# Performance work log

Hardware: AMD Instinct MI355X
Metric: run time of the kernel (lower is better)

Reference implementation:

```python
import jax, jax.numpy as jnp
import numpy as np

BETA_MAX = 0.01
CD_WEIGHT = 1.0
FIDELITY_WEIGHT = 0.5
BETA = BETA_MAX  # fully annealed (step >= beta_warmup)
EPS = 1e-12


def _pairwise_dist(a, b):
    """Euclidean distance matrix. a: [B,N,3], b: [B,M,3] -> [B,N,M]."""
    a2 = jnp.sum(a * a, axis=-1)                      # [B,N]
    b2 = jnp.sum(b * b, axis=-1)                      # [B,M]
    ab = jnp.einsum('bnd,bmd->bnm', a, b)             # [B,N,M]
    sq = a2[:, :, None] + b2[:, None, :] - 2.0 * ab
    return jnp.sqrt(jnp.maximum(sq, EPS))


def chamfer_distance_l1(pred, full):
    d = _pairwise_dist(pred, full)                    # [B,N,M]
    d_pf = jnp.min(d, axis=2)                         # pred -> full, [B,N]
    d_fp = jnp.min(d, axis=1)                         # full -> pred, [B,M]
    return 0.5 * (jnp.mean(d_pf) + jnp.mean(d_fp))


def fidelity_loss(partial, pred):
    # one-directional: every partial point should have a close predicted point
    d = _pairwise_dist(partial, pred)                 # [B,P,N]
    return jnp.mean(jnp.min(d, axis=2))


def kl_divergence(mu, logvar):
    # -0.5 * E_batch[ sum_dim (1 + logvar - mu^2 - exp(logvar)) ]
    kl = -0.5 * jnp.sum(1.0 + logvar - mu * mu - jnp.exp(logvar), axis=1)
    return jnp.mean(kl)


def setup_inputs() -> dict:
    key = jax.random.key(0)
    k1, k2, k3, k4, k5 = jax.random.split(key, 5)
    B, N, P, D = 8, 8192, 2048, 512
    return {
        'pred': jax.random.normal(k1, (B, N, 3), dtype=jnp.float32),
        'full': jax.random.normal(k2, (B, N, 3), dtype=jnp.float32),
        'partial': jax.random.normal(k3, (B, P, 3), dtype=jnp.float32),
        'mu': jax.random.normal(k4, (B, D), dtype=jnp.float32),
        'logvar': jax.random.normal(k5, (B, D), dtype=jnp.float32) * 0.1,
    }


def reference(pred, full, partial, mu, logvar):
    cd = chamfer_distance_l1(pred, full)
    kl = kl_divergence(mu, logvar)
    fidel = fidelity_loss(partial, pred)
    total = CD_WEIGHT * cd + BETA * kl + FIDELITY_WEIGHT * fidel
    return (total, cd, kl, fidel)
```

## Files before the change

### kernel.cpp

```cpp
#include <hip/hip_runtime.h>
#include <math.h>

#define BATCH 8
#define NPTS  8192
#define PPTS  2048
#define DLAT  512

typedef __attribute__((ext_vector_type(8)))  short short8;
typedef __attribute__((ext_vector_type(16))) float floatx16;

#define SEG      (2 * BATCH * NPTS + BATCH * PPTS)
#define DIR_PF   0
#define DIR_FP   (BATCH * NPTS)
#define DIR_FID  (2 * BATCH * NPTS)
#define OFF_SEG  8

#define CHUNK  1024
#define XBLK   512

__device__ __forceinline__ unsigned short f2bf(float f) {
    unsigned int u = __float_as_uint(f);
    return (unsigned short)((u + 0x7FFFu + ((u >> 16) & 1u)) >> 16);
}
__device__ __forceinline__ float bf2f(unsigned short s) {
    return __uint_as_float(((unsigned int)s) << 16);
}

__device__ __forceinline__ float min16(floatx16 d, float prev) {
    float a0 = fminf(fminf(d[0],  d[1]),  d[2]);
    float a1 = fminf(fminf(d[3],  d[4]),  d[5]);
    float a2 = fminf(fminf(d[6],  d[7]),  d[8]);
    float a3 = fminf(fminf(d[9],  d[10]), d[11]);
    float a4 = fminf(fminf(d[12], d[13]), d[14]);
    float b0 = fminf(fminf(a0, a1), a2);
    float b1 = fminf(fminf(a3, a4), d[15]);
    return fminf(fminf(b0, b1), prev);
}

__device__ __forceinline__ void encodeY(float y0, float y1, float y2,
                                        uint4* r0, uint4* r1) {
    const unsigned short h0 = f2bf(y0), h1 = f2bf(y1), h2 = f2bf(y2);
    const unsigned short l0 = f2bf(y0 - bf2f(h0));
    const unsigned short l1 = f2bf(y1 - bf2f(h1));
    const unsigned short l2 = f2bf(y2 - bf2f(h2));
    const float yn = fmaf(y0, y0, fmaf(y1, y1, y2 * y2));
    const unsigned short nh = f2bf(yn);
    const unsigned short nl = f2bf(yn - bf2f(nh));
    r0->x = (unsigned int)h0 | ((unsigned int)h1 << 16);
    r0->y = (unsigned int)h2 | ((unsigned int)l0 << 16);
    r0->z = (unsigned int)l1 | ((unsigned int)l2 << 16);
    r0->w = (unsigned int)h0 | ((unsigned int)h1 << 16);
    r1->x = (unsigned int)h2 | ((unsigned int)nh << 16);
    r1->y = (unsigned int)nl;
    r1->z = 0u; r1->w = 0u;
}

__global__ __launch_bounds__(256, 3) void minpass_kernel(
        const float* __restrict__ pred,
        const float* __restrict__ full,
        const float* __restrict__ partial,
        float* __restrict__ wsf,
        int ysplit) {
    const int bid = blockIdx.x;
    const int ys  = bid % ysplit;
    const int r   = bid / ysplit;
    const int b   = r / 36;
    const int s   = r % 36;
    const int yhalf = NPTS / ysplit;

    const int t = threadIdx.x;

    if (bid == 0) {
        if (t < 4) wsf[t] = 0.0f;
        if (t == 4) ((unsigned int*)wsf)[4] = 0u;
    }

    const float* xset; const float* yset; int minoff; int xbase;
    if (s < 16)      { xset = pred;    yset = full; xbase = b*NPTS + s*XBLK;
                       minoff = OFF_SEG + ys*SEG + DIR_PF  + b*NPTS + s*XBLK; }
    else if (s < 32) { xset = full;    yset = pred; xbase = b*NPTS + (s-16)*XBLK;
                       minoff = OFF_SEG + ys*SEG + DIR_FP  + b*NPTS + (s-16)*XBLK; }
    else             { xset = partial; yset = pred; xbase = b*PPTS + (s-32)*XBLK;
                       minoff = OFF_SEG + ys*SEG + DIR_FID + b*PPTS + (s-32)*XBLK; }

    const int lane = t & 63;
    const int wid  = t >> 6;
    const int l31  = lane & 31;
    const int half = lane >> 5;

    __shared__ uint4 sY[2][CHUNK];
    __shared__ uint4 sX[2][XBLK];
    __shared__ float sXn[XBLK];

    for (int i = t; i < XBLK; i += 256) {
        const float* xp = xset + (size_t)(xbase + i) * 3;
        const float x0 = xp[0], x1 = xp[1], x2 = xp[2];
        const float m0 = -2.0f*x0, m1 = -2.0f*x1, m2 = -2.0f*x2;
        const unsigned short h0 = f2bf(m0), h1 = f2bf(m1), h2 = f2bf(m2);
        const unsigned short l0 = f2bf(m0 - bf2f(h0));
        const unsigned short l1 = f2bf(m1 - bf2f(h1));
        const unsigned short l2 = f2bf(m2 - bf2f(h2));
        const unsigned int one = 0x3F80u;
        uint4 r0, r1;
        r0.x = (unsigned int)h0 | ((unsigned int)h1 << 16);
        r0.y = (unsigned int)h2 | ((unsigned int)h0 << 16);
        r0.z = (unsigned int)h1 | ((unsigned int)h2 << 16);
        r0.w = (unsigned int)l0 | ((unsigned int)l1 << 16);
        r1.x = (unsigned int)l2 | (one << 16);
        r1.y = one;
        r1.z = 0u; r1.w = 0u;
        sX[0][i] = r0; sX[1][i] = r1;
        sXn[i] = fmaf(x0, x0, fmaf(x1, x1, x2 * x2));
    }

    {
        const float* ypts = yset + (size_t)(b * NPTS + ys * yhalf) * 3;
        for (int i = t; i < CHUNK; i += 256) {
            const float* yp = ypts + (size_t)i * 3;
            uint4 r0, r1;
            encodeY(yp[0], yp[1], yp[2], &r0, &r1);
            sY[0][i] = r0; sY[1][i] = r1;
        }
    }
    __syncthreads();

    const int xw = wid * 128;
    const short8 bf0 = *(const short8*)&sX[half][xw + l31];
    const short8 bf1 = *(const short8*)&sX[half][xw + 32 + l31];
    const short8 bf2 = *(const short8*)&sX[half][xw + 64 + l31];
    const short8 bf3 = *(const short8*)&sX[half][xw + 96 + l31];
    const float  xn0 = sXn[xw + l31];
    const float  xn1 = sXn[xw + 32 + l31];
    const float  xn2 = sXn[xw + 64 + l31];
    const float  xn3 = sXn[xw + 96 + l31];

    const floatx16 zc = {0,0,0,0, 0,0,0,0, 0,0,0,0, 0,0,0,0};
    float cmin0 = 3.4e38f, cmin1 = 3.4e38f, cmin2 = 3.4e38f, cmin3 = 3.4e38f;

    const uint4* sYh = &sY[half][0];
    short8 af = *(const short8*)&sYh[l31];
#pragma unroll 4
    for (int j = 0; j < CHUNK / 32; ++j) {
        const short8 afn = *(const short8*)&sYh[((j + 1) & (CHUNK/32 - 1)) * 32 + l31];
        const floatx16 d0 = __builtin_amdgcn_mfma_f32_32x32x16_bf16(af, bf0, zc, 0, 0, 0);
        const floatx16 d1 = __builtin_amdgcn_mfma_f32_32x32x16_bf16(af, bf1, zc, 0, 0, 0);
        cmin0 = min16(d0, cmin0);
        const floatx16 d2 = __builtin_amdgcn_mfma_f32_32x32x16_bf16(af, bf2, zc, 0, 0, 0);
        cmin1 = min16(d1, cmin1);
        const floatx16 d3 = __builtin_amdgcn_mfma_f32_32x32x16_bf16(af, bf3, zc, 0, 0, 0);
        cmin2 = min16(d2, cmin2);
        cmin3 = min16(d3, cmin3);
        af = afn;
    }

    const float m0 = fminf(cmin0, __shfl_xor(cmin0, 32, 64));
    const float m1 = fminf(cmin1, __shfl_xor(cmin1, 32, 64));
    const float m2 = fminf(cmin2, __shfl_xor(cmin2, 32, 64));
    const float m3 = fminf(cmin3, __shfl_xor(cmin3, 32, 64));
    if (lane < 32) {
        wsf[minoff + xw + l31]      = fmaxf(m0 + xn0, 0.0f);
        wsf[minoff + xw + 32 + l31] = fmaxf(m1 + xn1, 0.0f);
        wsf[minoff + xw + 64 + l31] = fmaxf(m2 + xn2, 0.0f);
        wsf[minoff + xw + 96 + l31] = fmaxf(m3 + xn3, 0.0f);
    }
}

__device__ __forceinline__ float waveReduceSum(float v) {
#pragma unroll
    for (int o = 32; o > 0; o >>= 1) v += __shfl_down(v, o, 64);
    return v;
}

__device__ __forceinline__ float blockReduceSum(float v) {
    __shared__ float wsum[4];
    const int lane = threadIdx.x & 63;
    const int wid  = threadIdx.x >> 6;
    v = waveReduceSum(v);
    if (lane == 0) wsum[wid] = v;
    __syncthreads();
    if (wid == 0) {
        v = (lane < ((int)blockDim.x >> 6)) ? wsum[lane] : 0.0f;
        v = waveReduceSum(v);
    }
    return v;
}

#define NRED_BLOCKS 145
__global__ __launch_bounds__(256) void reduce_finalize_kernel(
        float* __restrict__ wsf,
        const float* __restrict__ mu,
        const float* __restrict__ logvar,
        float* __restrict__ out,
        int ysplit) {
    float* acc = wsf;
    unsigned int* cnt = (unsigned int*)wsf + 4;
    const int bid = blockIdx.x;
    const int t   = threadIdx.x;

    float v = 0.0f;
    int accIdx;
    if (bid < 144) {
        int base;
        if (bid < 64)       { accIdx = 0; base = DIR_PF  + bid * 1024;         }
        else if (bid < 128) { accIdx = 1; base = DIR_FP  + (bid - 64) * 1024;  }
        else                { accIdx = 2; base = DIR_FID + (bid - 128) * 1024; }
#pragma unroll
        for (int k = 0; k < 4; ++k) {
            const int i = OFF_SEG + base + k * 256 + t;
            float m = wsf[i];
            for (int sg = 1; sg < ysplit; ++sg) m = fminf(m, wsf[sg * SEG + i]);
            v += sqrtf(fmaxf(m, 1e-12f));
        }
    } else {
        accIdx = 3;
#pragma unroll
        for (int k = 0; k < BATCH * DLAT / 256; ++k) {
            const int i = k * 256 + t;
            const float m = mu[i];
            const float l = logvar[i];
            v += -0.5f * (1.0f + l - m * m - expf(l));
        }
    }

    v = blockReduceSum(v);
    if (t == 0) {
        atomicAdd(&acc[accIdx], v);
        __threadfence();
        const unsigned int done = atomicAdd(cnt, 1u);
        if (done == NRED_BLOCKS - 1) {
            const float s_pf  = atomicAdd(&acc[0], 0.0f);
            const float s_fp  = atomicAdd(&acc[1], 0.0f);
            const float s_fid = atomicAdd(&acc[2], 0.0f);
            const float s_kl  = atomicAdd(&acc[3], 0.0f);
            const float cd  = 0.5f * (s_pf / (float)(BATCH * NPTS) +
                                      s_fp / (float)(BATCH * NPTS));
            const float fid = s_fid / (float)(BATCH * PPTS);
            const float kl  = s_kl / (float)BATCH;
            out[0] = cd + 0.01f * kl + 0.5f * fid;
            out[1] = cd;
            out[2] = kl;
            out[3] = fid;
        }
    }
}

extern "C" void kernel_launch(void* const* d_in, const int* in_sizes, int n_in,
                              void* d_out, int out_size, void* d_ws, size_t ws_size,
                              hipStream_t stream) {
    const float* pred    = (const float*)d_in[0];
    const float* full    = (const float*)d_in[1];
    const float* partial = (const float*)d_in[2];
    const float* mu      = (const float*)d_in[3];
    const float* logvar  = (const float*)d_in[4];
    float* out = (float*)d_out;
    float* wsf = (float*)d_ws;

    int ysplit = 2;
    if (ws_size >= (size_t)(OFF_SEG + 8 * SEG) * 4) ysplit = 8;
    else if (ws_size >= (size_t)(OFF_SEG + 4 * SEG) * 4) ysplit = 4;

    minpass_kernel<<<8 * 36 * ysplit, 256, 0, stream>>>(pred, full, partial, wsf, ysplit);

    reduce_finalize_kernel<<<NRED_BLOCKS, 256, 0, stream>>>(wsf, mu, logvar, out, ysplit);
}
```

Before: 109.7 us.

## Switch to 16x16x32 bf16 MFMA with 8 x-tiles per wave and y-chunk loop

Replaces the 32x32x16 MFMA tiling with 16x16x32 MFMAs. Each wave now holds 8 x-fragments of 16 points, and the low-order bf16 terms are packed into the second K half so all 32 K slots carry data. The y dimension is now processed in a loop over CHUNK-sized tiles with syncs, so ysplit can be smaller than NPTS/CHUNK and more y work is done per block. The min reduction takes 4 outputs per MFMA instead of 16, which lowers the reduction VALU work per MFMA. The cost is more MFMA issues, zero-padded lanes for quads 2 and 3, and extra barriers per chunk.

```diff
diff --git a/kernel.cpp b/kernel.cpp
--- a/kernel.cpp
+++ b/kernel.cpp
@@ -6,8 +6,8 @@
 #define PPTS  2048
 #define DLAT  512
 
-typedef __attribute__((ext_vector_type(8)))  short short8;
-typedef __attribute__((ext_vector_type(16))) float floatx16;
+typedef __attribute__((ext_vector_type(8))) short short8;
+typedef __attribute__((ext_vector_type(4))) float floatx4;
 
 #define SEG      (2 * BATCH * NPTS + BATCH * PPTS)
 #define DIR_PF   0
@@ -26,16 +26,6 @@
     return __uint_as_float(((unsigned int)s) << 16);
 }
 
-__device__ __forceinline__ float min16(floatx16 d, float prev) {
-    float a0 = fminf(fminf(d[0],  d[1]),  d[2]);
-    float a1 = fminf(fminf(d[3],  d[4]),  d[5]);
-    float a2 = fminf(fminf(d[6],  d[7]),  d[8]);
-    float a3 = fminf(fminf(d[9],  d[10]), d[11]);
-    float a4 = fminf(fminf(d[12], d[13]), d[14]);
-    float b0 = fminf(fminf(a0, a1), a2);
-    float b1 = fminf(fminf(a3, a4), d[15]);
-    return fminf(fminf(b0, b1), prev);
-}
 
 __device__ __forceinline__ void encodeY(float y0, float y1, float y2,
                                         uint4* r0, uint4* r1) {
@@ -51,8 +41,9 @@
     r0->z = (unsigned int)l1 | ((unsigned int)l2 << 16);
     r0->w = (unsigned int)h0 | ((unsigned int)h1 << 16);
     r1->x = (unsigned int)h2 | ((unsigned int)nh << 16);
-    r1->y = (unsigned int)nl;
-    r1->z = 0u; r1->w = 0u;
+    r1->y = (unsigned int)nl | ((unsigned int)l0 << 16);
+    r1->z = (unsigned int)l1 | ((unsigned int)l2 << 16);
+    r1->w = 0u;
 }
 
 __global__ __launch_bounds__(256, 3) void minpass_kernel(
@@ -85,8 +76,9 @@
 
     const int lane = t & 63;
     const int wid  = t >> 6;
-    const int l31  = lane & 31;
-    const int half = lane >> 5;
+    const int m    = lane & 15;
+    const int quad = lane >> 4;
+    const int qh   = quad & 1;
 
     __shared__ uint4 sY[2][CHUNK];
     __shared__ uint4 sX[2][XBLK];
@@ -107,61 +99,65 @@
         r0.z = (unsigned int)h1 | ((unsigned int)h2 << 16);
         r0.w = (unsigned int)l0 | ((unsigned int)l1 << 16);
         r1.x = (unsigned int)l2 | (one << 16);
-        r1.y = one;
-        r1.z = 0u; r1.w = 0u;
+        r1.y = one | ((unsigned int)l0 << 16);
+        r1.z = (unsigned int)l1 | ((unsigned int)l2 << 16);
+        r1.w = 0u;
         sX[0][i] = r0; sX[1][i] = r1;
         sXn[i] = fmaf(x0, x0, fmaf(x1, x1, x2 * x2));
     }
-
-    {
-        const float* ypts = yset + (size_t)(b * NPTS + ys * yhalf) * 3;
+    __syncthreads();
+
+    const int xw = wid * 128;
+    short8 bf[8];
+    float  xn[8];
+#pragma unroll
+    for (int i = 0; i < 8; ++i) {
+        short8 v = {0, 0, 0, 0, 0, 0, 0, 0};
+        if (quad < 2) v = *(const short8*)&sX[qh][xw + i * 16 + m];
+        bf[i] = v;
+        xn[i] = sXn[xw + i * 16 + m];
+    }
+
+    const floatx4 zc = {0.0f, 0.0f, 0.0f, 0.0f};
+    float cmin[8];
+#pragma unroll
+    for (int i = 0; i < 8; ++i) cmin[i] = 3.4e38f;
+
+    const float* yptsBase = yset + (size_t)(b * NPTS + ys * yhalf) * 3;
+
+    for (int c = 0; c < yhalf; c += CHUNK) {
+        __syncthreads();
         for (int i = t; i < CHUNK; i += 256) {
-            const float* yp = ypts + (size_t)i * 3;
+            const float* yp = yptsBase + (size_t)(c + i) * 3;
             uint4 r0, r1;
             encodeY(yp[0], yp[1], yp[2], &r0, &r1);
             sY[0][i] = r0; sY[1][i] = r1;
         }
-    }
-    __syncthreads();
-
-    const int xw = wid * 128;
-    const short8 bf0 = *(const short8*)&sX[half][xw + l31];
-    const short8 bf1 = *(const short8*)&sX[half][xw + 32 + l31];
-    const short8 bf2 = *(const short8*)&sX[half][xw + 64 + l31];
-    const short8 bf3 = *(const short8*)&sX[half][xw + 96 + l31];
-    const float  xn0 = sXn[xw + l31];
-    const float  xn1 = sXn[xw + 32 + l31];
-    const float  xn2 = sXn[xw + 64 + l31];
-    const float  xn3 = sXn[xw + 96 + l31];
-
-    const floatx16 zc = {0,0,0,0, 0,0,0,0, 0,0,0,0, 0,0,0,0};
-    float cmin0 = 3.4e38f, cmin1 = 3.4e38f, cmin2 = 3.4e38f, cmin3 = 3.4e38f;
-
-    const uint4* sYh = &sY[half][0];
-    short8 af = *(const short8*)&sYh[l31];
+        __syncthreads();
+
+        short8 af = *(const short8*)&sY[qh][m];
 #pragma unroll 4
-    for (int j = 0; j < CHUNK / 32; ++j) {
-        const short8 afn = *(const short8*)&sYh[((j + 1) & (CHUNK/32 - 1)) * 32 + l31];
-        const floatx16 d0 = __builtin_amdgcn_mfma_f32_32x32x16_bf16(af, bf0, zc, 0, 0, 0);
-        const floatx16 d1 = __builtin_amdgcn_mfma_f32_32x32x16_bf16(af, bf1, zc, 0, 0, 0);
-        cmin0 = min16(d0, cmin0);
-        const floatx16 d2 = __builtin_amdgcn_mfma_f32_32x32x16_bf16(af, bf2, zc, 0, 0, 0);
-        cmin1 = min16(d1, cmin1);
-        const floatx16 d3 = __builtin_amdgcn_mfma_f32_32x32x16_bf16(af, bf3, zc, 0, 0, 0);
-        cmin2 = min16(d2, cmin2);
-        cmin3 = min16(d3, cmin3);
-        af = afn;
-    }
-
-    const float m0 = fminf(cmin0, __shfl_xor(cmin0, 32, 64));
-    const float m1 = fminf(cmin1, __shfl_xor(cmin1, 32, 64));
-    const float m2 = fminf(cmin2, __shfl_xor(cmin2, 32, 64));
-    const float m3 = fminf(cmin3, __shfl_xor(cmin3, 32, 64));
-    if (lane < 32) {
-        wsf[minoff + xw + l31]      = fmaxf(m0 + xn0, 0.0f);
-        wsf[minoff + xw + 32 + l31] = fmaxf(m1 + xn1, 0.0f);
-        wsf[minoff + xw + 64 + l31] = fmaxf(m2 + xn2, 0.0f);
-        wsf[minoff + xw + 96 + l31] = fmaxf(m3 + xn3, 0.0f);
+        for (int j = 0; j < CHUNK / 16; ++j) {
+            const short8 afn =
+                *(const short8*)&sY[qh][((j + 1) & (CHUNK / 16 - 1)) * 16 + m];
+#pragma unroll
+            for (int i = 0; i < 8; ++i) {
+                const floatx4 d =
+                    __builtin_amdgcn_mfma_f32_16x16x32_bf16(af, bf[i], zc, 0, 0, 0);
+                const float t3 = fminf(fminf(d[0], d[1]), d[2]);
+                cmin[i] = fminf(fminf(d[3], t3), cmin[i]);
+            }
+            af = afn;
+        }
+    }
+
+#pragma unroll
+    for (int i = 0; i < 8; ++i) {
+        float v = cmin[i];
+        v = fminf(v, __shfl_xor(v, 16, 64));
+        v = fminf(v, __shfl_xor(v, 32, 64));
+        if (lane < 16)
+            wsf[minoff + xw + i * 16 + m] = fmaxf(v + xn[i], 0.0f);
     }
 }
 
@@ -207,9 +203,10 @@
 #pragma unroll
         for (int k = 0; k < 4; ++k) {
             const int i = OFF_SEG + base + k * 256 + t;
-            float m = wsf[i];
-            for (int sg = 1; sg < ysplit; ++sg) m = fminf(m, wsf[sg * SEG + i]);
-            v += sqrtf(fmaxf(m, 1e-12f));
+            float mval = wsf[i];
+            for (int sg = 1; sg < ysplit; ++sg)
+                mval = fminf(mval, wsf[sg * SEG + i]);
+            v += sqrtf(fmaxf(mval, 1e-12f));
         }
     } else {
         accIdx = 3;
```

New measurement: 128.2 us. 16.9% more time.
